# Optimization experiments

Hardware: AMD Instinct MI355X
Metric: run time of the kernel (lower is better)

Reference implementation:

```python
import jax, jax.numpy as jnp
import numpy as np

HEADS = 8
DIM_HEAD = 64
INNER = HEADS * DIM_HEAD  # 512
QUERY_DIM = 512
CONTEXT_DIM = 512


def setup_inputs() -> dict:
    key = jax.random.key(0)
    ks = jax.random.split(key, 10)
    s_in = 1.0 / np.sqrt(QUERY_DIM)
    s_ctx = 1.0 / np.sqrt(CONTEXT_DIM)
    s_o = 1.0 / np.sqrt(INNER)
    return {
        "x": jax.random.normal(ks[0], (8, QUERY_DIM, 32, 32), jnp.float32),
        "context": jax.random.normal(ks[1], (8, CONTEXT_DIM, 32, 32), jnp.float32),
        "Wq": jax.random.normal(ks[2], (INNER, QUERY_DIM), jnp.float32) * s_in,
        "bq": jnp.zeros((INNER,), jnp.float32),
        "Wk": jax.random.normal(ks[3], (INNER, CONTEXT_DIM), jnp.float32) * s_ctx,
        "bk": jnp.zeros((INNER,), jnp.float32),
        "Wv": jax.random.normal(ks[4], (INNER, CONTEXT_DIM), jnp.float32) * s_ctx,
        "bv": jnp.zeros((INNER,), jnp.float32),
        "Wo": jax.random.normal(ks[5], (QUERY_DIM, INNER), jnp.float32) * s_o,
        "bo": jnp.zeros((QUERY_DIM,), jnp.float32),
    }


def _proj1x1(t, W, b):
    # 1x1 Conv2d: channel mixing only. t: [B,Cin,X,Y], W: [Cout,Cin]
    return jnp.einsum('bcxy,oc->boxy', t, W) + b[None, :, None, None]


def reference(x, context, Wq, bq, Wk, bk, Wv, bv, Wo, bo):
    b, c, h, w = x.shape
    scale = DIM_HEAD ** (-0.5)

    q = _proj1x1(x, Wq, bq)
    k = _proj1x1(context, Wk, bk)
    v = _proj1x1(context, Wv, bv)

    def split_heads(t):
        B, C, X, Y = t.shape  # C = HEADS*DIM_HEAD
        return t.reshape(B, HEADS, DIM_HEAD, X * Y)  # b h d n

    q = split_heads(q) * scale
    k = split_heads(k)
    v = split_heads(v)

    sim = jnp.einsum('bhdi,bhdj->bhij', q, k)          # [b,h,i,j]
    attn = jax.nn.softmax(sim, axis=-1)
    out = jnp.einsum('bhij,bhdj->bhid', attn, v)       # [b,h,i,d]
    # rearrange 'b h (x y) d -> b (h d) x y'
    out = out.transpose(0, 1, 3, 2).reshape(b, HEADS * DIM_HEAD, h, w)
    return _proj1x1(out, Wo, bo)
```

## Files before the change

kernel.cpp:

```cpp
#include <hip/hip_runtime.h>
#include <stdint.h>

#define NB   8
#define CH   512
#define NPIX 1024
#define DH   64

typedef float  f32x4  __attribute__((ext_vector_type(4)));
typedef float  f32x16 __attribute__((ext_vector_type(16)));
typedef __bf16 bf16x8 __attribute__((ext_vector_type(8)));
typedef unsigned int u32x4 __attribute__((ext_vector_type(4)));

static __device__ __forceinline__ unsigned short f2bf(float f) {
    unsigned int u = __builtin_bit_cast(unsigned int, f);
    u += 0x7FFFu + ((u >> 16) & 1u);
    return (unsigned short)(u >> 16);
}

static __device__ __forceinline__ bf16x8 ld_bf8(const unsigned short* p) {
    return *reinterpret_cast<const bf16x8*>(p);
}

static __device__ __forceinline__ unsigned int cvtpk_bf16(float lo, float hi) {
    unsigned int r;
    asm("v_cvt_pk_bf16_f32 %0,%1,%2" : "=v"(r) : "v"(lo), "v"(hi));
    return r;
}

static __device__ __forceinline__ void plswap(unsigned int& a, unsigned int& b) {
    asm("v_permlane32_swap_b32 %0, %1" : "+v"(a), "+v"(b));
}

static __device__ __forceinline__ void glds16(const unsigned short* g, void* l) {
    __builtin_amdgcn_global_load_lds(
        (const __attribute__((address_space(1))) unsigned int*)g,
        (__attribute__((address_space(3))) unsigned int*)l,
        16, 0, 0);
}

#define WAIT_VMCNT_8() asm volatile("s_waitcnt vmcnt(8)" ::: "memory")
#define WAIT_VMCNT_4() asm volatile("s_waitcnt vmcnt(4)" ::: "memory")
#define WAIT_VMCNT_0() asm volatile("s_waitcnt vmcnt(0)" ::: "memory")
#define WAIT_LGKM_0()  asm volatile("s_waitcnt lgkmcnt(0)" ::: "memory")

__global__ __launch_bounds__(256) void wconv_kernel(
        const float* __restrict__ Wq, const float* __restrict__ Wk,
        const float* __restrict__ Wv, const float* __restrict__ Wo,
        unsigned short* __restrict__ out) {
    int idx = blockIdx.x * 256 + threadIdx.x;
    int which = idx >> 18;
    int off   = idx & 0x3FFFF;
    const float* src = which == 0 ? Wq : which == 1 ? Wk : which == 2 ? Wv : Wo;
    out[idx] = f2bf(src[off]);
}

__global__ __launch_bounds__(256) void tconv_kernel(
        const float* __restrict__ x, const float* __restrict__ ctx,
        unsigned short* __restrict__ XT, unsigned short* __restrict__ CT) {
    __shared__ float tile[32][33];
    const int z = blockIdx.z;
    const float* src = (z < 8) ? x : ctx;
    unsigned short* dst = (z < 8) ? XT : CT;
    const int b  = z & 7;
    const int c0 = blockIdx.x * 32, n0 = blockIdx.y * 32;
    const int tx = threadIdx.x, ty = threadIdx.y;
    const float* s = src + (size_t)b * CH * NPIX;
#pragma unroll
    for (int i = 0; i < 4; i++) {
        int r = i * 8 + ty;
        tile[r][tx] = s[(size_t)(c0 + r) * NPIX + n0 + tx];
    }
    __syncthreads();
    unsigned short* d = dst + (size_t)b * NPIX * CH;
#pragma unroll
    for (int i = 0; i < 4; i++) {
        int r = i * 8 + ty;
        d[(size_t)(n0 + r) * CH + c0 + tx] = f2bf(tile[tx][r]);
    }
}

static __device__ __forceinline__ void gemm128(
        const unsigned short* __restrict__ Wp,
        const unsigned short* __restrict__ Xp,
        f32x4 acc[4][4]) {
    __shared__ __align__(16) unsigned short lA[2][128][32];
    __shared__ __align__(16) unsigned short lB[2][128][32];
    const int tid  = threadIdx.x;
    const int lane = tid & 63;
    const int wv   = tid >> 6;
    const int wm   = wv & 1, wn = tid >> 7;

    const unsigned short* gA = Wp + (size_t)(wv * 32 + (lane >> 2)) * CH + (lane & 3) * 8;
    const unsigned short* gB = Xp + (size_t)(wv * 32 + (lane >> 2)) * CH + (lane & 3) * 8;

    auto stage = [&](int kt, int buf) {
        const int k0 = kt * 32;
        char* dA = (char*)&lA[buf][0][0] + wv * 2048;
        char* dB = (char*)&lB[buf][0][0] + wv * 2048;
        glds16(gA + k0,           dA);
        glds16(gA + k0 + 16 * CH, dA + 1024);
        glds16(gB + k0,           dB);
        glds16(gB + k0 + 16 * CH, dB + 1024);
    };

    stage(0, 0);
    stage(1, 1);

#pragma unroll 1
    for (int kt = 0; kt < 16; kt++) {
        if (kt < 15) { WAIT_VMCNT_4(); } else { WAIT_VMCNT_0(); }
        __builtin_amdgcn_s_barrier();
        const int buf = kt & 1;
        bf16x8 af[4], bfrag[4];
#pragma unroll
        for (int i = 0; i < 4; i++)
            af[i] = ld_bf8(&lA[buf][wm * 64 + i * 16 + (lane & 15)][(lane >> 4) * 8]);
#pragma unroll
        for (int j = 0; j < 4; j++)
            bfrag[j] = ld_bf8(&lB[buf][wn * 64 + j * 16 + (lane & 15)][(lane >> 4) * 8]);
#pragma unroll
        for (int i = 0; i < 4; i++)
#pragma unroll
            for (int j = 0; j < 4; j++)
                acc[i][j] = __builtin_amdgcn_mfma_f32_16x16x32_bf16(af[i], bfrag[j], acc[i][j], 0, 0, 0);
        WAIT_LGKM_0();
        __builtin_amdgcn_s_barrier();
        if (kt + 2 < 16) stage(kt + 2, buf);
    }
}

__global__ __launch_bounds__(256) void proj_qkv_kernel(
        const unsigned short* __restrict__ XT, const unsigned short* __restrict__ CT,
        const unsigned short* __restrict__ Wbf,
        const float* __restrict__ bq, const float* __restrict__ bk, const float* __restrict__ bv,
        unsigned short* __restrict__ Q, unsigned short* __restrict__ K, unsigned short* __restrict__ V) {
    const int z = blockIdx.z;
    const int b = z / 3, mode = z - 3 * b;
    const int o0 = blockIdx.x * 128, n0 = blockIdx.y * 128;
    const unsigned short* W = Wbf + (size_t)mode * CH * CH;
    const unsigned short* X = (mode == 0 ? XT : CT) + (size_t)b * NPIX * CH;
    const float* bias = mode == 0 ? bq : mode == 1 ? bk : bv;

    f32x4 acc[4][4];
#pragma unroll
    for (int i = 0; i < 4; i++)
#pragma unroll
        for (int j = 0; j < 4; j++)
#pragma unroll
            for (int r = 0; r < 4; r++) acc[i][j][r] = 0.f;

    gemm128(W + (size_t)o0 * CH, X + (size_t)n0 * CH, acc);

    const int lane = threadIdx.x & 63;
    const int wm = (threadIdx.x >> 6) & 1, wn = threadIdx.x >> 7;
    const float qs = 0.125f * 1.44269504088896340736f;
#pragma unroll
    for (int i = 0; i < 4; i++) {
        const int ob = o0 + wm * 64 + i * 16 + (lane >> 4) * 4;
        const int h = ob >> 6, dd = ob & 63;
        float b4[4];
#pragma unroll
        for (int r = 0; r < 4; r++) b4[r] = bias[ob + r];
#pragma unroll
        for (int j = 0; j < 4; j++) {
            const int n = n0 + wn * 64 + j * 16 + (lane & 15);
            float v[4];
#pragma unroll
            for (int r = 0; r < 4; r++) v[r] = acc[i][j][r] + b4[r];
            if (mode == 0) {
#pragma unroll
                for (int r = 0; r < 4; r++) v[r] *= qs;
            }
            if (mode <= 1) {
                unsigned int lo = (unsigned)f2bf(v[0]) | ((unsigned)f2bf(v[1]) << 16);
                unsigned int hi = (unsigned)f2bf(v[2]) | ((unsigned)f2bf(v[3]) << 16);
                unsigned short* dst = (mode == 0 ? Q : K) +
                    (((size_t)(b * 8 + h) * NPIX) + n) * DH + dd;
                *(uint2*)dst = make_uint2(lo, hi);
            } else {
#pragma unroll
                for (int r = 0; r < 4; r++)
                    V[((((size_t)(b * 8 + h) * 16) + (n >> 6)) * 64 + dd + r) * 64 + (n & 63)]
                        = f2bf(v[r]);
            }
        }
    }
}

__global__ __launch_bounds__(128) void attn_kernel(
        const unsigned short* __restrict__ Qg, const unsigned short* __restrict__ Kg,
        const unsigned short* __restrict__ Vg, unsigned short* __restrict__ AT) {
    __shared__ __align__(16) unsigned short ldsK[2][4096];
    __shared__ __align__(16) unsigned short ldsV[2][4096];

    const int p  = blockIdx.x;
    const int w  = p >> 3;
    const int bh = ((p & 7) << 3) | (w >> 4);
    const int qb = w & 15;
    const int q0 = qb * 64;
    const int tid = threadIdx.x, wave = tid >> 6, lane = tid & 63;
    const int lq = lane & 31, hi = lane >> 5, lql = lq & 7;

    const unsigned short* Qb = Qg + ((size_t)bh * NPIX + q0 + wave * 32 + lq) * DH + hi * 8;
    bf16x8 qf[4];
#pragma unroll
    for (int ds = 0; ds < 4; ds++) qf[ds] = ld_bf8(Qb + ds * 16);

    f32x16 o0, o1;
#pragma unroll
    for (int r = 0; r < 16; r++) { o0[r] = 0.f; o1[r] = 0.f; }
    float l_run = 0.f;

    const int swz = (((lane & 7) ^ ((lane >> 3) & 7)) << 3);
    const unsigned short* gsrc = (wave == 0)
        ? Kg + ((size_t)bh * NPIX + (lane >> 3)) * DH + swz
        : Vg + (((size_t)bh * 16 * 64) + (lane >> 3)) * 64 + swz;
    char* ldsbase0 = (char*)(wave == 0 ? &ldsK[0][0] : &ldsV[0][0]);
    char* ldsbase1 = (char*)(wave == 0 ? &ldsK[1][0] : &ldsV[1][0]);

    auto stage = [&](int tile, char* dst) {
        const unsigned short* s0 = gsrc + (size_t)tile * 4096;
#pragma unroll
        for (int i = 0; i < 8; i++)
            glds16(s0 + i * 512, dst + i * 1024);
    };

    stage(0, ldsbase0);
    stage(1, ldsbase1);

#pragma unroll 1
    for (int t = 0; t < 16; ++t) {
        if (t < 15) { WAIT_VMCNT_8(); } else { WAIT_VMCNT_0(); }
        __builtin_amdgcn_s_barrier();
        const int cur = t & 1;
        const unsigned short* kbuf = &ldsK[cur][0];
        const unsigned short* vbuf = &ldsV[cur][0];
#pragma unroll
        for (int st = 0; st < 2; ++st) {
            const unsigned short* kb = kbuf + (st * 32 + lq) * 64;
            bf16x8 kf0 = ld_bf8(kb + (((0 + hi) ^ lql) << 3));
            bf16x8 kf1 = ld_bf8(kb + (((2 + hi) ^ lql) << 3));
            bf16x8 kf2 = ld_bf8(kb + (((4 + hi) ^ lql) << 3));
            bf16x8 kf3 = ld_bf8(kb + (((6 + hi) ^ lql) << 3));

            f32x16 s;
#pragma unroll
            for (int r = 0; r < 16; r++) s[r] = 0.f;
            __builtin_amdgcn_s_setprio(1);
            s = __builtin_amdgcn_mfma_f32_32x32x16_bf16(kf0, qf[0], s, 0, 0, 0);
            s = __builtin_amdgcn_mfma_f32_32x32x16_bf16(kf1, qf[1], s, 0, 0, 0);
            s = __builtin_amdgcn_mfma_f32_32x32x16_bf16(kf2, qf[2], s, 0, 0, 0);
            s = __builtin_amdgcn_mfma_f32_32x32x16_bf16(kf3, qf[3], s, 0, 0, 0);
            __builtin_amdgcn_s_setprio(0);

            const unsigned short* vb0 = vbuf + lq * 64;
            const unsigned short* vb1 = vbuf + (32 + lq) * 64;
            bf16x8 v00 = ld_bf8(vb0 + (((st * 4 + 0 + hi) ^ lql) << 3));
            bf16x8 v01 = ld_bf8(vb0 + (((st * 4 + 2 + hi) ^ lql) << 3));
            bf16x8 v10 = ld_bf8(vb1 + (((st * 4 + 0 + hi) ^ lql) << 3));
            bf16x8 v11 = ld_bf8(vb1 + (((st * 4 + 2 + hi) ^ lql) << 3));

#pragma unroll
            for (int r = 0; r < 16; r++) s[r] = exp2f(s[r]);
            float s8[8], s4[4];
#pragma unroll
            for (int i = 0; i < 8; i++) s8[i] = s[2 * i] + s[2 * i + 1];
#pragma unroll
            for (int i = 0; i < 4; i++) s4[i] = s8[2 * i] + s8[2 * i + 1];
            l_run += (s4[0] + s4[1]) + (s4[2] + s4[3]);

            bf16x8 pa[2];
#pragma unroll
            for (int ks = 0; ks < 2; ks++) {
                const int bse = ks * 8;
                unsigned int X0 = cvtpk_bf16(s[bse + 0], s[bse + 1]);
                unsigned int X1 = cvtpk_bf16(s[bse + 2], s[bse + 3]);
                unsigned int X2 = cvtpk_bf16(s[bse + 4], s[bse + 5]);
                unsigned int X3 = cvtpk_bf16(s[bse + 6], s[bse + 7]);
                plswap(X0, X2); plswap(X1, X3);
                u32x4 wv; wv[0] = X0; wv[1] = X1; wv[2] = X2; wv[3] = X3;
                pa[ks] = __builtin_bit_cast(bf16x8, wv);
            }

            __builtin_amdgcn_s_setprio(1);
            o0 = __builtin_amdgcn_mfma_f32_32x32x16_bf16(pa[0], v00, o0, 0, 0, 0);
            o1 = __builtin_amdgcn_mfma_f32_32x32x16_bf16(pa[0], v10, o1, 0, 0, 0);
            o0 = __builtin_amdgcn_mfma_f32_32x32x16_bf16(pa[1], v01, o0, 0, 0, 0);
            o1 = __builtin_amdgcn_mfma_f32_32x32x16_bf16(pa[1], v11, o1, 0, 0, 0);
            __builtin_amdgcn_s_setprio(0);
        }
        WAIT_LGKM_0();
        __builtin_amdgcn_s_barrier();
        if (t + 2 < 16)
            stage(t + 2, cur ? ldsbase1 : ldsbase0);
    }

    l_run += __shfl_xor(l_run, 32);
    float inv = 1.0f / l_run;
    const int b = bh >> 3, h = bh & 7;
#pragma unroll
    for (int r = 0; r < 16; r++) {
        int crow = (r & 3) + 8 * (r >> 2) + 4 * hi;
        float fac = __shfl(inv, crow);
        int q = q0 + wave * 32 + crow;
        unsigned short* dst = AT + ((size_t)b * NPIX + q) * CH + h * 64 + lq;
        dst[0]  = f2bf(o0[r] * fac);
        dst[32] = f2bf(o1[r] * fac);
    }
}

__global__ __launch_bounds__(256) void proj_out_kernel(
        const unsigned short* __restrict__ AT, const unsigned short* __restrict__ Wo,
        const float* __restrict__ bo, float* __restrict__ out) {
    const int b = blockIdx.z;
    const int o0 = blockIdx.x * 128, n0 = blockIdx.y * 128;
    f32x4 acc[4][4];
#pragma unroll
    for (int i = 0; i < 4; i++)
#pragma unroll
        for (int j = 0; j < 4; j++)
#pragma unroll
            for (int r = 0; r < 4; r++) acc[i][j][r] = 0.f;

    gemm128(Wo + (size_t)o0 * CH, AT + ((size_t)b * NPIX + n0) * CH, acc);

    const int lane = threadIdx.x & 63;
    const int wm = (threadIdx.x >> 6) & 1, wn = threadIdx.x >> 7;
#pragma unroll
    for (int i = 0; i < 4; i++) {
        const int ob = o0 + wm * 64 + i * 16 + (lane >> 4) * 4;
        float b4[4];
#pragma unroll
        for (int r = 0; r < 4; r++) b4[r] = bo[ob + r];
#pragma unroll
        for (int j = 0; j < 4; j++) {
            const int n = n0 + wn * 64 + j * 16 + (lane & 15);
#pragma unroll
            for (int r = 0; r < 4; r++)
                out[((size_t)b * CH + ob + r) * NPIX + n] = acc[i][j][r] + b4[r];
        }
    }
}

extern "C" void kernel_launch(void* const* d_in, const int* in_sizes, int n_in,
                              void* d_out, int out_size, void* d_ws, size_t ws_size,
                              hipStream_t stream) {
    const float* x   = (const float*)d_in[0];
    const float* ctx = (const float*)d_in[1];
    const float* Wq  = (const float*)d_in[2];
    const float* bq  = (const float*)d_in[3];
    const float* Wk  = (const float*)d_in[4];
    const float* bk  = (const float*)d_in[5];
    const float* Wv  = (const float*)d_in[6];
    const float* bv  = (const float*)d_in[7];
    const float* Wo  = (const float*)d_in[8];
    const float* bo  = (const float*)d_in[9];
    float* out = (float*)d_out;

    char* ws = (char*)d_ws;
    unsigned short* XT  = (unsigned short*)(ws);
    unsigned short* CT  = (unsigned short*)(ws + 8388608);
    unsigned short* Wbf = (unsigned short*)(ws + 16777216);
    unsigned short* Q   = (unsigned short*)(ws + 18874368);
    unsigned short* K   = (unsigned short*)(ws + 27262976);
    unsigned short* V   = (unsigned short*)(ws + 35651584);
    unsigned short* AT  = XT;

    wconv_kernel<<<4096, 256, 0, stream>>>(Wq, Wk, Wv, Wo, Wbf);
    tconv_kernel<<<dim3(16, 32, 16), dim3(32, 8), 0, stream>>>(x, ctx, XT, CT);
    proj_qkv_kernel<<<dim3(4, 8, 24), 256, 0, stream>>>(XT, CT, Wbf, bq, bk, bv, Q, K, V);
    attn_kernel<<<1024, 128, 0, stream>>>(Q, K, V, AT);
    proj_out_kernel<<<dim3(4, 8, 8), 256, 0, stream>>>(AT, Wbf + 3 * 262144, bo, out);
}
```

Before: 96.68 us.

## Restructure attention into single-wave blocks, vectorize transpose, use raw v_exp

The attention kernel becomes one wave per 32-query block with 32-key tiles. Each lane stages both K and V, so the cross-wave barriers go away, and the V layout is reshaped into 32-pixel tiles to match. The grid doubles to 2048 blocks for more parallelism. exp2f is replaced by raw v_exp_f32, and the input transpose kernel now uses float4 loads and packed bf16 stores with 256 flat threads. This trades more loop iterations and more K/Q reloads per key for lower sync overhead and higher occupancy.

```diff
diff --git a/kernel.cpp b/kernel.cpp
--- a/kernel.cpp
+++ b/kernel.cpp
@@ -24,6 +24,12 @@
 static __device__ __forceinline__ unsigned int cvtpk_bf16(float lo, float hi) {
     unsigned int r;
     asm("v_cvt_pk_bf16_f32 %0,%1,%2" : "=v"(r) : "v"(lo), "v"(hi));
+    return r;
+}
+
+static __device__ __forceinline__ float fexp2(float x) {
+    float r;
+    asm("v_exp_f32 %0, %1" : "=v"(r) : "v"(x));
     return r;
 }
 
@@ -63,20 +69,17 @@
     unsigned short* dst = (z < 8) ? XT : CT;
     const int b  = z & 7;
     const int c0 = blockIdx.x * 32, n0 = blockIdx.y * 32;
-    const int tx = threadIdx.x, ty = threadIdx.y;
-    const float* s = src + (size_t)b * CH * NPIX;
-#pragma unroll
-    for (int i = 0; i < 4; i++) {
-        int r = i * 8 + ty;
-        tile[r][tx] = s[(size_t)(c0 + r) * NPIX + n0 + tx];
-    }
+    const int t  = threadIdx.x;
+    const int r  = t >> 3, ch4 = (t & 7) * 4;
+    const float* s = src + (size_t)b * CH * NPIX + (size_t)(c0 + r) * NPIX + n0 + ch4;
+    float4 v4 = *(const float4*)s;
+    tile[r][ch4] = v4.x; tile[r][ch4 + 1] = v4.y;
+    tile[r][ch4 + 2] = v4.z; tile[r][ch4 + 3] = v4.w;
     __syncthreads();
-    unsigned short* d = dst + (size_t)b * NPIX * CH;
-#pragma unroll
-    for (int i = 0; i < 4; i++) {
-        int r = i * 8 + ty;
-        d[(size_t)(n0 + r) * CH + c0 + tx] = f2bf(tile[tx][r]);
-    }
+    unsigned int lo = ((unsigned)f2bf(tile[ch4 + 1][r]) << 16) | f2bf(tile[ch4][r]);
+    unsigned int hw = ((unsigned)f2bf(tile[ch4 + 3][r]) << 16) | f2bf(tile[ch4 + 2][r]);
+    *(uint2*)(dst + (size_t)b * NPIX * CH + (size_t)(n0 + r) * CH + c0 + ch4)
+        = make_uint2(lo, hw);
 }
 
 static __device__ __forceinline__ void gemm128(
@@ -180,119 +183,117 @@
             } else {
 #pragma unroll
                 for (int r = 0; r < 4; r++)
-                    V[((((size_t)(b * 8 + h) * 16) + (n >> 6)) * 64 + dd + r) * 64 + (n & 63)]
+                    V[(((size_t)(b * 8 + h) * 32 + (n >> 5)) * 64 + dd + r) * 32 + (n & 31)]
                         = f2bf(v[r]);
             }
         }
     }
 }
 
-__global__ __launch_bounds__(128) void attn_kernel(
+__global__ __launch_bounds__(64) void attn_kernel(
         const unsigned short* __restrict__ Qg, const unsigned short* __restrict__ Kg,
         const unsigned short* __restrict__ Vg, unsigned short* __restrict__ AT) {
-    __shared__ __align__(16) unsigned short ldsK[2][4096];
-    __shared__ __align__(16) unsigned short ldsV[2][4096];
+    __shared__ __align__(16) unsigned short ldsK[2][2048];
+    __shared__ __align__(16) unsigned short ldsV[2][2048];
 
     const int p  = blockIdx.x;
-    const int w  = p >> 3;
-    const int bh = ((p & 7) << 3) | (w >> 4);
-    const int qb = w & 15;
-    const int q0 = qb * 64;
-    const int tid = threadIdx.x, wave = tid >> 6, lane = tid & 63;
-    const int lq = lane & 31, hi = lane >> 5, lql = lq & 7;
-
-    const unsigned short* Qb = Qg + ((size_t)bh * NPIX + q0 + wave * 32 + lq) * DH + hi * 8;
+    const int local = p >> 3;
+    const int bh = ((p & 7) << 3) | (local >> 5);
+    const int qb = local & 31;
+    const int q0 = qb * 32;
+    const int lane = threadIdx.x;
+    const int lq = lane & 31, hi = lane >> 5;
+
+    const unsigned short* Qb = Qg + ((size_t)bh * NPIX + q0 + lq) * DH + hi * 8;
     bf16x8 qf[4];
 #pragma unroll
     for (int ds = 0; ds < 4; ds++) qf[ds] = ld_bf8(Qb + ds * 16);
 
-    f32x16 o0, o1;
-#pragma unroll
-    for (int r = 0; r < 16; r++) { o0[r] = 0.f; o1[r] = 0.f; }
+    f32x16 o0, o1, zro;
+#pragma unroll
+    for (int r = 0; r < 16; r++) { o0[r] = 0.f; o1[r] = 0.f; zro[r] = 0.f; }
     float l_run = 0.f;
 
-    const int swz = (((lane & 7) ^ ((lane >> 3) & 7)) << 3);
-    const unsigned short* gsrc = (wave == 0)
-        ? Kg + ((size_t)bh * NPIX + (lane >> 3)) * DH + swz
-        : Vg + (((size_t)bh * 16 * 64) + (lane >> 3)) * 64 + swz;
-    char* ldsbase0 = (char*)(wave == 0 ? &ldsK[0][0] : &ldsV[0][0]);
-    char* ldsbase1 = (char*)(wave == 0 ? &ldsK[1][0] : &ldsV[1][0]);
-
-    auto stage = [&](int tile, char* dst) {
-        const unsigned short* s0 = gsrc + (size_t)tile * 4096;
-#pragma unroll
-        for (int i = 0; i < 8; i++)
-            glds16(s0 + i * 512, dst + i * 1024);
+    const int swzK = (((lane & 7) ^ ((lane >> 3) & 7)) << 3);
+    const unsigned short* gK = Kg + ((size_t)bh * NPIX + (lane >> 3)) * DH + swzK;
+    const int swzV = (((lane & 3) ^ ((lane >> 2) & 3)) << 3);
+    const unsigned short* gV = Vg + (size_t)bh * 32 * 2048 + (size_t)(lane >> 2) * 32 + swzV;
+
+    auto stage = [&](int t, int buf) {
+        const unsigned short* sk = gK + (size_t)t * 32 * DH;
+        char* dK = (char*)&ldsK[buf][0];
+        glds16(sk,           dK);
+        glds16(sk +  8 * DH, dK + 1024);
+        glds16(sk + 16 * DH, dK + 2048);
+        glds16(sk + 24 * DH, dK + 3072);
+        const unsigned short* sv = gV + (size_t)t * 2048;
+        char* dV = (char*)&ldsV[buf][0];
+        glds16(sv,        dV);
+        glds16(sv +  512, dV + 1024);
+        glds16(sv + 1024, dV + 2048);
+        glds16(sv + 1536, dV + 3072);
     };
 
-    stage(0, ldsbase0);
-    stage(1, ldsbase1);
-
+    stage(0, 0);
+    stage(1, 1);
+
+    const int lql7 = lq & 7, lql3 = lq & 3;
 #pragma unroll 1
-    for (int t = 0; t < 16; ++t) {
-        if (t < 15) { WAIT_VMCNT_8(); } else { WAIT_VMCNT_0(); }
-        __builtin_amdgcn_s_barrier();
+    for (int t = 0; t < 32; ++t) {
+        if (t < 31) { WAIT_VMCNT_8(); } else { WAIT_VMCNT_0(); }
         const int cur = t & 1;
-        const unsigned short* kbuf = &ldsK[cur][0];
-        const unsigned short* vbuf = &ldsV[cur][0];
-#pragma unroll
-        for (int st = 0; st < 2; ++st) {
-            const unsigned short* kb = kbuf + (st * 32 + lq) * 64;
-            bf16x8 kf0 = ld_bf8(kb + (((0 + hi) ^ lql) << 3));
-            bf16x8 kf1 = ld_bf8(kb + (((2 + hi) ^ lql) << 3));
-            bf16x8 kf2 = ld_bf8(kb + (((4 + hi) ^ lql) << 3));
-            bf16x8 kf3 = ld_bf8(kb + (((6 + hi) ^ lql) << 3));
-
-            f32x16 s;
-#pragma unroll
-            for (int r = 0; r < 16; r++) s[r] = 0.f;
-            __builtin_amdgcn_s_setprio(1);
-            s = __builtin_amdgcn_mfma_f32_32x32x16_bf16(kf0, qf[0], s, 0, 0, 0);
-            s = __builtin_amdgcn_mfma_f32_32x32x16_bf16(kf1, qf[1], s, 0, 0, 0);
-            s = __builtin_amdgcn_mfma_f32_32x32x16_bf16(kf2, qf[2], s, 0, 0, 0);
-            s = __builtin_amdgcn_mfma_f32_32x32x16_bf16(kf3, qf[3], s, 0, 0, 0);
-            __builtin_amdgcn_s_setprio(0);
-
-            const unsigned short* vb0 = vbuf + lq * 64;
-            const unsigned short* vb1 = vbuf + (32 + lq) * 64;
-            bf16x8 v00 = ld_bf8(vb0 + (((st * 4 + 0 + hi) ^ lql) << 3));
-            bf16x8 v01 = ld_bf8(vb0 + (((st * 4 + 2 + hi) ^ lql) << 3));
-            bf16x8 v10 = ld_bf8(vb1 + (((st * 4 + 0 + hi) ^ lql) << 3));
-            bf16x8 v11 = ld_bf8(vb1 + (((st * 4 + 2 + hi) ^ lql) << 3));
-
-#pragma unroll
-            for (int r = 0; r < 16; r++) s[r] = exp2f(s[r]);
-            float s8[8], s4[4];
-#pragma unroll
-            for (int i = 0; i < 8; i++) s8[i] = s[2 * i] + s[2 * i + 1];
-#pragma unroll
-            for (int i = 0; i < 4; i++) s4[i] = s8[2 * i] + s8[2 * i + 1];
-            l_run += (s4[0] + s4[1]) + (s4[2] + s4[3]);
-
-            bf16x8 pa[2];
-#pragma unroll
-            for (int ks = 0; ks < 2; ks++) {
-                const int bse = ks * 8;
-                unsigned int X0 = cvtpk_bf16(s[bse + 0], s[bse + 1]);
-                unsigned int X1 = cvtpk_bf16(s[bse + 2], s[bse + 3]);
-                unsigned int X2 = cvtpk_bf16(s[bse + 4], s[bse + 5]);
-                unsigned int X3 = cvtpk_bf16(s[bse + 6], s[bse + 7]);
-                plswap(X0, X2); plswap(X1, X3);
-                u32x4 wv; wv[0] = X0; wv[1] = X1; wv[2] = X2; wv[3] = X3;
-                pa[ks] = __builtin_bit_cast(bf16x8, wv);
-            }
-
-            __builtin_amdgcn_s_setprio(1);
-            o0 = __builtin_amdgcn_mfma_f32_32x32x16_bf16(pa[0], v00, o0, 0, 0, 0);
-            o1 = __builtin_amdgcn_mfma_f32_32x32x16_bf16(pa[0], v10, o1, 0, 0, 0);
-            o0 = __builtin_amdgcn_mfma_f32_32x32x16_bf16(pa[1], v01, o0, 0, 0, 0);
-            o1 = __builtin_amdgcn_mfma_f32_32x32x16_bf16(pa[1], v11, o1, 0, 0, 0);
-            __builtin_amdgcn_s_setprio(0);
+        const unsigned short* kb = &ldsK[cur][0] + lq * 64;
+        bf16x8 kf0 = ld_bf8(kb + (((0 + hi) ^ lql7) << 3));
+        bf16x8 kf1 = ld_bf8(kb + (((2 + hi) ^ lql7) << 3));
+        bf16x8 kf2 = ld_bf8(kb + (((4 + hi) ^ lql7) << 3));
+        bf16x8 kf3 = ld_bf8(kb + (((6 + hi) ^ lql7) << 3));
+
+        f32x16 s;
+        __builtin_amdgcn_s_setprio(1);
+        s = __builtin_amdgcn_mfma_f32_32x32x16_bf16(kf0, qf[0], zro, 0, 0, 0);
+        s = __builtin_amdgcn_mfma_f32_32x32x16_bf16(kf1, qf[1], s, 0, 0, 0);
+        s = __builtin_amdgcn_mfma_f32_32x32x16_bf16(kf2, qf[2], s, 0, 0, 0);
+        s = __builtin_amdgcn_mfma_f32_32x32x16_bf16(kf3, qf[3], s, 0, 0, 0);
+        __builtin_amdgcn_s_setprio(0);
+
+        const unsigned short* vb0 = &ldsV[cur][0] + lq * 32;
+        const unsigned short* vb1 = vb0 + 32 * 32;
+        bf16x8 v00 = ld_bf8(vb0 + (((0 + hi) ^ lql3) << 3));
+        bf16x8 v01 = ld_bf8(vb0 + (((2 + hi) ^ lql3) << 3));
+        bf16x8 v10 = ld_bf8(vb1 + (((0 + hi) ^ lql3) << 3));
+        bf16x8 v11 = ld_bf8(vb1 + (((2 + hi) ^ lql3) << 3));
+
+#pragma unroll
+        for (int r = 0; r < 16; r++) s[r] = fexp2(s[r]);
+        float s8[8], s4[4];
+#pragma unroll
+        for (int i = 0; i < 8; i++) s8[i] = s[2 * i] + s[2 * i + 1];
+#pragma unroll
+        for (int i = 0; i < 4; i++) s4[i] = s8[2 * i] + s8[2 * i + 1];
+        l_run += (s4[0] + s4[1]) + (s4[2] + s4[3]);
+
+        bf16x8 pa[2];
+#pragma unroll
+        for (int ks = 0; ks < 2; ks++) {
+            const int bse = ks * 8;
+            unsigned int X0 = cvtpk_bf16(s[bse + 0], s[bse + 1]);
+            unsigned int X1 = cvtpk_bf16(s[bse + 2], s[bse + 3]);
+            unsigned int X2 = cvtpk_bf16(s[bse + 4], s[bse + 5]);
+            unsigned int X3 = cvtpk_bf16(s[bse + 6], s[bse + 7]);
+            plswap(X0, X2); plswap(X1, X3);
+            u32x4 wv; wv[0] = X0; wv[1] = X1; wv[2] = X2; wv[3] = X3;
+            pa[ks] = __builtin_bit_cast(bf16x8, wv);
         }
-        WAIT_LGKM_0();
-        __builtin_amdgcn_s_barrier();
-        if (t + 2 < 16)
-            stage(t + 2, cur ? ldsbase1 : ldsbase0);
+
+        __builtin_amdgcn_s_setprio(1);
+        o0 = __builtin_amdgcn_mfma_f32_32x32x16_bf16(pa[0], v00, o0, 0, 0, 0);
+        o1 = __builtin_amdgcn_mfma_f32_32x32x16_bf16(pa[0], v10, o1, 0, 0, 0);
+        o0 = __builtin_amdgcn_mfma_f32_32x32x16_bf16(pa[1], v01, o0, 0, 0, 0);
+        o1 = __builtin_amdgcn_mfma_f32_32x32x16_bf16(pa[1], v11, o1, 0, 0, 0);
+        __builtin_amdgcn_s_setprio(0);
+
+        __builtin_amdgcn_sched_barrier(0);
+        if (t + 2 < 32) stage(t + 2, cur);
     }
 
     l_run += __shfl_xor(l_run, 32);
@@ -302,7 +303,7 @@
     for (int r = 0; r < 16; r++) {
         int crow = (r & 3) + 8 * (r >> 2) + 4 * hi;
         float fac = __shfl(inv, crow);
-        int q = q0 + wave * 32 + crow;
+        int q = q0 + crow;
         unsigned short* dst = AT + ((size_t)b * NPIX + q) * CH + h * 64 + lq;
         dst[0]  = f2bf(o0[r] * fac);
         dst[32] = f2bf(o1[r] * fac);
@@ -367,8 +368,8 @@
     unsigned short* AT  = XT;
 
     wconv_kernel<<<4096, 256, 0, stream>>>(Wq, Wk, Wv, Wo, Wbf);
-    tconv_kernel<<<dim3(16, 32, 16), dim3(32, 8), 0, stream>>>(x, ctx, XT, CT);
+    tconv_kernel<<<dim3(16, 32, 16), 256, 0, stream>>>(x, ctx, XT, CT);
     proj_qkv_kernel<<<dim3(4, 8, 24), 256, 0, stream>>>(XT, CT, Wbf, bq, bk, bv, Q, K, V);
-    attn_kernel<<<1024, 128, 0, stream>>>(Q, K, V, AT);
+    attn_kernel<<<2048, 64, 0, stream>>>(Q, K, V, AT);
     proj_out_kernel<<<dim3(4, 8, 8), 256, 0, stream>>>(AT, Wbf + 3 * 262144, bo, out);
 }
```

Measured after the change: 94.23 us. 1.03x faster.
